# Performance work log

Measured on AMD Instinct MI355X. Metric: run time of the kernel, lower is better.

## Reference

```python
import jax, jax.numpy as jnp
import numpy as np

C = 1.0                      # Poincare ball curvature (pmath.project k=1.0)
SQRT_C = jnp.float32(np.sqrt(C))
MIN_NORM = 1e-15
BALL_EPS = 4e-3              # geoopt float32 boundary eps


def _norm(x):
    return jnp.clip(jnp.linalg.norm(x, axis=-1, keepdims=True), MIN_NORM, None)


def _artanh(x):
    return jnp.arctanh(jnp.clip(x, -1 + 1e-7, 1 - 1e-7))


def logmap0(x):
    # tangent vector at origin: artanh(sqrt(c)||x||) * x / (sqrt(c)||x||)
    n = _norm(x)
    return _artanh(SQRT_C * n) * x / (SQRT_C * n)


def expmap0(u):
    # point on ball: tanh(sqrt(c)||u||) * u / (sqrt(c)||u||)
    n = _norm(u)
    return jnp.tanh(SQRT_C * n) * u / (SQRT_C * n)


def project(x):
    # clip to open ball of radius (1-eps)/sqrt(c)
    n = _norm(x)
    maxnorm = (1.0 - BALL_EPS) / SQRT_C
    return jnp.where(n > maxnorm, x * (maxnorm / n), x)


def setup_inputs() -> dict:
    key = jax.random.key(0)
    k1, k2 = jax.random.split(key)
    B, N, D = 2, 8192, 256
    # valid Poincare-ball points: small tangent vectors mapped onto the ball
    x = project(expmap0(0.1 * jax.random.normal(k1, (B, N, D), dtype=jnp.float32)))
    # row-normalized-ish dense adjacency standing in for the sparse adj
    adj = jax.random.uniform(k2, (B, N, N), dtype=jnp.float32) / N
    return {"x": x, "adj": adj}


def reference(x, adj) -> jnp.ndarray:
    # HypAgg.forward: aggregate in tangent space at origin, map back, project
    x_tangent = logmap0(x)                          # [B, N, D]
    support_t = jnp.einsum("bij,bjd->bid", adj, x_tangent)  # batched spmm
    return project(expmap0(support_t))              # [B, N, D]
```

## Files before the change

### kernel.cpp

```cpp
#include <hip/hip_runtime.h>

#define BATCH 2
#define NN 8192
#define DD 256
#define BK 64

typedef __attribute__((ext_vector_type(8))) short bf16x8;
typedef __attribute__((ext_vector_type(4))) float f32x4;

__device__ __forceinline__ unsigned short f2bf(float f) {
    unsigned u = __builtin_bit_cast(unsigned, f);
    u += 0x7fffu + ((u >> 16) & 1u);
    return (unsigned short)(u >> 16);
}

__global__ void k_logmap_scale(const float* __restrict__ x, float* __restrict__ scale) {
    int row = blockIdx.x;
    int lane = threadIdx.x;
    const float4* xr = (const float4*)(x + (size_t)row * DD);
    float4 v = xr[lane];
    float s = v.x * v.x + v.y * v.y + v.z * v.z + v.w * v.w;
#pragma unroll
    for (int m = 1; m < 64; m <<= 1) s += __shfl_xor(s, m, 64);
    if (lane == 0) {
        float n = sqrtf(s);
        n = fmaxf(n, 1e-15f);
        float z = fminf(n, 1.0f - 1e-7f);
        float at = 0.5f * logf((1.0f + z) / (1.0f - z));
        scale[row] = at / n;
    }
}

__global__ void k_transpose(const float* __restrict__ x, const float* __restrict__ scale,
                            unsigned short* __restrict__ xtf) {
    __shared__ __align__(16) unsigned short T[DD][72];
    int bid = blockIdx.x;
    int b = bid >> 7, kb = bid & 127;
    int bn0 = b * NN + kb * 64;
    int t = threadIdx.x;
    int r = t >> 2, cc = t & 3;
    float sc = scale[bn0 + r];
    const float4* rp = (const float4*)(x + (size_t)(bn0 + r) * DD + cc * 64);
#pragma unroll
    for (int j4 = 0; j4 < 16; ++j4) {
        float4 v = rp[j4];
        int d = cc * 64 + j4 * 4;
        T[d + 0][r] = f2bf(v.x * sc);
        T[d + 1][r] = f2bf(v.y * sc);
        T[d + 2][r] = f2bf(v.z * sc);
        T[d + 3][r] = f2bf(v.w * sc);
    }
    __syncthreads();
    unsigned short* outp = xtf + (size_t)(b * 128 + kb) * DD * 64;
    int dd = t >> 3, ccc = t & 7;
#pragma unroll
    for (int p = 0; p < 8; ++p) {
        int d = dd + 32 * p;
        bf16x8 val = *(const bf16x8*)&T[d][ccc * 8];
        *(bf16x8*)(outp + (size_t)d * 64 + ccc * 8) = val;
    }
}

__global__ __launch_bounds__(256, 1) void k_gemm(const float* __restrict__ adj,
                                                 const unsigned short* __restrict__ xtf,
                                                 float* __restrict__ out) {
    __shared__ __align__(16) unsigned short A_lds[64][72];
    __shared__ float red[4][64];
    __shared__ float rowscale[64];

    int bid = blockIdx.x;
    int xcd = bid & 7;
    int b = xcd >> 2;
    int mtile = ((bid >> 3) << 2) | (xcd & 3);
    int m0 = mtile * 64;

    int t = threadIdx.x;
    int w = t >> 6, lane = t & 63, c = lane & 15, q = lane >> 4;

    int ar = t >> 4;
    int ac4 = t & 15;
    const float* abase = adj + (size_t)b * NN * NN + (size_t)(m0 + ar) * NN + ac4 * 4;

    const unsigned short* xbase = xtf + (size_t)b * 128 * DD * 64
                                + (size_t)(w * 64 + c) * 64 + q * 8;

    f32x4 acc[4][4];
#pragma unroll
    for (int i = 0; i < 4; ++i)
#pragma unroll
        for (int j = 0; j < 4; ++j)
#pragma unroll
            for (int rg = 0; rg < 4; ++rg) acc[i][j][rg] = 0.0f;

    float4 av[4];
    bf16x8 bcur[4][2], bnxt[4][2];

#pragma unroll
    for (int i = 0; i < 4; ++i)
        av[i] = *(const float4*)(abase + (size_t)(i * 16) * NN);
#pragma unroll
    for (int nt = 0; nt < 4; ++nt)
#pragma unroll
        for (int kk = 0; kk < 2; ++kk)
            bcur[nt][kk] = *(const bf16x8*)(xbase + nt * 16 * 64 + kk * 32);

    for (int kb = 0; kb < 128; ++kb) {
#pragma unroll
        for (int i = 0; i < 4; ++i) {
            ushort4 pk;
            pk.x = f2bf(av[i].x); pk.y = f2bf(av[i].y);
            pk.z = f2bf(av[i].z); pk.w = f2bf(av[i].w);
            *(ushort4*)&A_lds[ar + i * 16][ac4 * 4] = pk;
        }
        __syncthreads();

        if (kb + 1 < 128) {
            const float* ab = abase + (size_t)(kb + 1) * BK;
#pragma unroll
            for (int i = 0; i < 4; ++i)
                av[i] = *(const float4*)(ab + (size_t)(i * 16) * NN);
            const unsigned short* xb = xbase + (size_t)(kb + 1) * DD * 64;
#pragma unroll
            for (int nt = 0; nt < 4; ++nt)
#pragma unroll
                for (int kk = 0; kk < 2; ++kk)
                    bnxt[nt][kk] = *(const bf16x8*)(xb + nt * 16 * 64 + kk * 32);
        }

#pragma unroll
        for (int kk = 0; kk < 2; ++kk) {
            bf16x8 af[4];
#pragma unroll
            for (int mt = 0; mt < 4; ++mt)
                af[mt] = *(const bf16x8*)&A_lds[mt * 16 + c][kk * 32 + q * 8];
#pragma unroll
            for (int mt = 0; mt < 4; ++mt)
#pragma unroll
                for (int nt = 0; nt < 4; ++nt)
                    acc[mt][nt] = __builtin_amdgcn_mfma_f32_16x16x32_bf16(
                        af[mt], bcur[nt][kk], acc[mt][nt], 0, 0, 0);
        }
        __syncthreads();

        if (kb + 1 < 128) {
#pragma unroll
            for (int nt = 0; nt < 4; ++nt)
#pragma unroll
                for (int kk = 0; kk < 2; ++kk)
                    bcur[nt][kk] = bnxt[nt][kk];
        }
    }

    float s[4][4];
#pragma unroll
    for (int mt = 0; mt < 4; ++mt)
#pragma unroll
        for (int rg = 0; rg < 4; ++rg) {
            float v = acc[mt][0][rg] * acc[mt][0][rg] + acc[mt][1][rg] * acc[mt][1][rg]
                    + acc[mt][2][rg] * acc[mt][2][rg] + acc[mt][3][rg] * acc[mt][3][rg];
            v += __shfl_xor(v, 1, 64);
            v += __shfl_xor(v, 2, 64);
            v += __shfl_xor(v, 4, 64);
            v += __shfl_xor(v, 8, 64);
            s[mt][rg] = v;
        }
#pragma unroll
    for (int mt = 0; mt < 4; ++mt)
#pragma unroll
        for (int rg = 0; rg < 4; ++rg)
            if (c == mt * 4 + rg)
                red[w][mt * 16 + q * 4 + rg] = s[mt][rg];
    __syncthreads();
    if (t < 64) {
        float tot = red[0][t] + red[1][t] + red[2][t] + red[3][t];
        float n = sqrtf(tot);
        n = fmaxf(n, 1e-15f);
        float th = tanhf(n);
        rowscale[t] = fminf(th, 1.0f - 4e-3f) / n;
    }
    __syncthreads();

    float* obase = out + ((size_t)b * NN + m0) * DD + w * 64 + c;
#pragma unroll
    for (int mt = 0; mt < 4; ++mt)
#pragma unroll
        for (int rg = 0; rg < 4; ++rg) {
            float rs = rowscale[mt * 16 + q * 4 + rg];
            float* orow = obase + (size_t)(mt * 16 + q * 4 + rg) * DD;
#pragma unroll
            for (int nt = 0; nt < 4; ++nt)
                orow[nt * 16] = acc[mt][nt][rg] * rs;
        }
}

extern "C" void kernel_launch(void* const* d_in, const int* in_sizes, int n_in,
                              void* d_out, int out_size, void* d_ws, size_t ws_size,
                              hipStream_t stream) {
    const float* x   = (const float*)d_in[0];
    const float* adj = (const float*)d_in[1];
    float* out = (float*)d_out;

    unsigned short* xtf = (unsigned short*)d_ws;
    float* scale = (float*)((char*)d_ws + (size_t)BATCH * 128 * DD * 64 * 2);

    k_logmap_scale<<<BATCH * NN, 64, 0, stream>>>(x, scale);
    k_transpose<<<BATCH * 128, 256, 0, stream>>>(x, scale, xtf);
    k_gemm<<<256, 256, 0, stream>>>(adj, xtf, out);
}
```

Before: 801.6 us.

## Load adj directly into MFMA registers, drop LDS staging, fuse prep kernels

The GEMM no longer stages the fp32 adjacency tile through LDS with barriers. Each wave now loads its A fragments straight from global memory with nontemporal loads and converts them in registers. Waves are arranged 2x2 over a 32x128 sub-tile, and global loads are double-buffered in registers across two k-steps. The logmap norm and transpose kernels are merged into one prep kernel, and output stores are nontemporal. This removes the LDS round trips, barriers and one kernel launch, at the cost of more register pressure and less coalesced per-lane adj loads (32-byte segments per row).

```diff
diff --git a/kernel.cpp b/kernel.cpp
--- a/kernel.cpp
+++ b/kernel.cpp
@@ -3,7 +3,6 @@
 #define BATCH 2
 #define NN 8192
 #define DD 256
-#define BK 64
 
 typedef __attribute__((ext_vector_type(8))) short bf16x8;
 typedef __attribute__((ext_vector_type(4))) float f32x4;
@@ -14,41 +13,43 @@
     return (unsigned short)(u >> 16);
 }
 
-__global__ void k_logmap_scale(const float* __restrict__ x, float* __restrict__ scale) {
-    int row = blockIdx.x;
-    int lane = threadIdx.x;
-    const float4* xr = (const float4*)(x + (size_t)row * DD);
-    float4 v = xr[lane];
-    float s = v.x * v.x + v.y * v.y + v.z * v.z + v.w * v.w;
+__device__ __forceinline__ bf16x8 cvt8(f32x4 lo, f32x4 hi) {
+    bf16x8 r;
 #pragma unroll
-    for (int m = 1; m < 64; m <<= 1) s += __shfl_xor(s, m, 64);
-    if (lane == 0) {
-        float n = sqrtf(s);
-        n = fmaxf(n, 1e-15f);
-        float z = fminf(n, 1.0f - 1e-7f);
-        float at = 0.5f * logf((1.0f + z) / (1.0f - z));
-        scale[row] = at / n;
+    for (int i = 0; i < 4; ++i) {
+        r[i]     = (short)f2bf(lo[i]);
+        r[i + 4] = (short)f2bf(hi[i]);
     }
+    return r;
 }
 
-__global__ void k_transpose(const float* __restrict__ x, const float* __restrict__ scale,
-                            unsigned short* __restrict__ xtf) {
+__global__ void k_prep(const float* __restrict__ x, unsigned short* __restrict__ xtf) {
     __shared__ __align__(16) unsigned short T[DD][72];
     int bid = blockIdx.x;
     int b = bid >> 7, kb = bid & 127;
     int bn0 = b * NN + kb * 64;
     int t = threadIdx.x;
     int r = t >> 2, cc = t & 3;
-    float sc = scale[bn0 + r];
     const float4* rp = (const float4*)(x + (size_t)(bn0 + r) * DD + cc * 64);
+    float4 v[16];
+    float s = 0.0f;
 #pragma unroll
     for (int j4 = 0; j4 < 16; ++j4) {
-        float4 v = rp[j4];
+        v[j4] = rp[j4];
+        s += v[j4].x * v[j4].x + v[j4].y * v[j4].y + v[j4].z * v[j4].z + v[j4].w * v[j4].w;
+    }
+    s += __shfl_xor(s, 1, 64);
+    s += __shfl_xor(s, 2, 64);
+    float n = fmaxf(sqrtf(s), 1e-15f);
+    float z = fminf(n, 1.0f - 1e-7f);
+    float sc = (0.5f * logf((1.0f + z) / (1.0f - z))) / n;
+#pragma unroll
+    for (int j4 = 0; j4 < 16; ++j4) {
         int d = cc * 64 + j4 * 4;
-        T[d + 0][r] = f2bf(v.x * sc);
-        T[d + 1][r] = f2bf(v.y * sc);
-        T[d + 2][r] = f2bf(v.z * sc);
-        T[d + 3][r] = f2bf(v.w * sc);
+        T[d + 0][r] = f2bf(v[j4].x * sc);
+        T[d + 1][r] = f2bf(v[j4].y * sc);
+        T[d + 2][r] = f2bf(v[j4].z * sc);
+        T[d + 3][r] = f2bf(v[j4].w * sc);
     }
     __syncthreads();
     unsigned short* outp = xtf + (size_t)(b * 128 + kb) * DD * 64;
@@ -61,11 +62,46 @@
     }
 }
 
+struct ABuf { f32x4 a[2][2][2]; };
+struct BBuf { bf16x8 f[8][2]; };
+
+__device__ __forceinline__ void load_tiles(const float* abase, const unsigned short* bbase,
+                                           int kb, ABuf& A, BBuf& B) {
+#pragma unroll
+    for (int mt = 0; mt < 2; ++mt)
+#pragma unroll
+        for (int kk = 0; kk < 2; ++kk) {
+            const f32x4* p = (const f32x4*)(abase + (size_t)mt * 16 * NN + (size_t)kb * 64 + kk * 32);
+            A.a[mt][kk][0] = __builtin_nontemporal_load(p);
+            A.a[mt][kk][1] = __builtin_nontemporal_load(p + 1);
+        }
+    const unsigned short* bk = bbase + (size_t)kb * DD * 64;
+#pragma unroll
+    for (int nt = 0; nt < 8; ++nt)
+#pragma unroll
+        for (int kk = 0; kk < 2; ++kk)
+            B.f[nt][kk] = *(const bf16x8*)(bk + nt * 16 * 64 + kk * 32);
+}
+
+__device__ __forceinline__ void compute_tiles(const ABuf& A, const BBuf& B, f32x4 acc[2][8]) {
+#pragma unroll
+    for (int kk = 0; kk < 2; ++kk) {
+        bf16x8 af[2];
+#pragma unroll
+        for (int mt = 0; mt < 2; ++mt) af[mt] = cvt8(A.a[mt][kk][0], A.a[mt][kk][1]);
+#pragma unroll
+        for (int mt = 0; mt < 2; ++mt)
+#pragma unroll
+            for (int nt = 0; nt < 8; ++nt)
+                acc[mt][nt] = __builtin_amdgcn_mfma_f32_16x16x32_bf16(
+                    af[mt], B.f[nt][kk], acc[mt][nt], 0, 0, 0);
+    }
+}
+
 __global__ __launch_bounds__(256, 1) void k_gemm(const float* __restrict__ adj,
                                                  const unsigned short* __restrict__ xtf,
                                                  float* __restrict__ out) {
-    __shared__ __align__(16) unsigned short A_lds[64][72];
-    __shared__ float red[4][64];
+    __shared__ float red[2][64];
     __shared__ float rowscale[64];
 
     int bid = blockIdx.x;
@@ -76,120 +112,62 @@
 
     int t = threadIdx.x;
     int w = t >> 6, lane = t & 63, c = lane & 15, q = lane >> 4;
+    int wm = w >> 1, wn = w & 1;
 
-    int ar = t >> 4;
-    int ac4 = t & 15;
-    const float* abase = adj + (size_t)b * NN * NN + (size_t)(m0 + ar) * NN + ac4 * 4;
+    const float* abase = adj + (size_t)b * NN * NN + (size_t)(m0 + wm * 32 + c) * NN + q * 8;
+    const unsigned short* bbase = xtf + (size_t)b * 128 * DD * 64
+                                + (size_t)(wn * 128 + c) * 64 + q * 8;
 
-    const unsigned short* xbase = xtf + (size_t)b * 128 * DD * 64
-                                + (size_t)(w * 64 + c) * 64 + q * 8;
+    f32x4 acc[2][8];
+#pragma unroll
+    for (int mt = 0; mt < 2; ++mt)
+#pragma unroll
+        for (int nt = 0; nt < 8; ++nt)
+#pragma unroll
+            for (int rg = 0; rg < 4; ++rg) acc[mt][nt][rg] = 0.0f;
 
-    f32x4 acc[4][4];
-#pragma unroll
-    for (int i = 0; i < 4; ++i)
-#pragma unroll
-        for (int j = 0; j < 4; ++j)
-#pragma unroll
-            for (int rg = 0; rg < 4; ++rg) acc[i][j][rg] = 0.0f;
-
-    float4 av[4];
-    bf16x8 bcur[4][2], bnxt[4][2];
+    ABuf A0, A1;
+    BBuf B0, B1;
+    load_tiles(abase, bbase, 0, A0, B0);
+    for (int kb = 0; kb < 128; kb += 2) {
+        load_tiles(abase, bbase, kb + 1, A1, B1);
+        compute_tiles(A0, B0, acc);
+        if (kb + 2 < 128) load_tiles(abase, bbase, kb + 2, A0, B0);
+        compute_tiles(A1, B1, acc);
+    }
 
 #pragma unroll
-    for (int i = 0; i < 4; ++i)
-        av[i] = *(const float4*)(abase + (size_t)(i * 16) * NN);
-#pragma unroll
-    for (int nt = 0; nt < 4; ++nt)
-#pragma unroll
-        for (int kk = 0; kk < 2; ++kk)
-            bcur[nt][kk] = *(const bf16x8*)(xbase + nt * 16 * 64 + kk * 32);
-
-    for (int kb = 0; kb < 128; ++kb) {
-#pragma unroll
-        for (int i = 0; i < 4; ++i) {
-            ushort4 pk;
-            pk.x = f2bf(av[i].x); pk.y = f2bf(av[i].y);
-            pk.z = f2bf(av[i].z); pk.w = f2bf(av[i].w);
-            *(ushort4*)&A_lds[ar + i * 16][ac4 * 4] = pk;
-        }
-        __syncthreads();
-
-        if (kb + 1 < 128) {
-            const float* ab = abase + (size_t)(kb + 1) * BK;
-#pragma unroll
-            for (int i = 0; i < 4; ++i)
-                av[i] = *(const float4*)(ab + (size_t)(i * 16) * NN);
-            const unsigned short* xb = xbase + (size_t)(kb + 1) * DD * 64;
-#pragma unroll
-            for (int nt = 0; nt < 4; ++nt)
-#pragma unroll
-                for (int kk = 0; kk < 2; ++kk)
-                    bnxt[nt][kk] = *(const bf16x8*)(xb + nt * 16 * 64 + kk * 32);
-        }
-
-#pragma unroll
-        for (int kk = 0; kk < 2; ++kk) {
-            bf16x8 af[4];
-#pragma unroll
-            for (int mt = 0; mt < 4; ++mt)
-                af[mt] = *(const bf16x8*)&A_lds[mt * 16 + c][kk * 32 + q * 8];
-#pragma unroll
-            for (int mt = 0; mt < 4; ++mt)
-#pragma unroll
-                for (int nt = 0; nt < 4; ++nt)
-                    acc[mt][nt] = __builtin_amdgcn_mfma_f32_16x16x32_bf16(
-                        af[mt], bcur[nt][kk], acc[mt][nt], 0, 0, 0);
-        }
-        __syncthreads();
-
-        if (kb + 1 < 128) {
-#pragma unroll
-            for (int nt = 0; nt < 4; ++nt)
-#pragma unroll
-                for (int kk = 0; kk < 2; ++kk)
-                    bcur[nt][kk] = bnxt[nt][kk];
-        }
-    }
-
-    float s[4][4];
-#pragma unroll
-    for (int mt = 0; mt < 4; ++mt)
+    for (int mt = 0; mt < 2; ++mt)
 #pragma unroll
         for (int rg = 0; rg < 4; ++rg) {
-            float v = acc[mt][0][rg] * acc[mt][0][rg] + acc[mt][1][rg] * acc[mt][1][rg]
-                    + acc[mt][2][rg] * acc[mt][2][rg] + acc[mt][3][rg] * acc[mt][3][rg];
+            float v = 0.0f;
+#pragma unroll
+            for (int nt = 0; nt < 8; ++nt) v += acc[mt][nt][rg] * acc[mt][nt][rg];
             v += __shfl_xor(v, 1, 64);
             v += __shfl_xor(v, 2, 64);
             v += __shfl_xor(v, 4, 64);
             v += __shfl_xor(v, 8, 64);
-            s[mt][rg] = v;
+            if (c == 0) red[wn][wm * 32 + mt * 16 + q * 4 + rg] = v;
         }
-#pragma unroll
-    for (int mt = 0; mt < 4; ++mt)
-#pragma unroll
-        for (int rg = 0; rg < 4; ++rg)
-            if (c == mt * 4 + rg)
-                red[w][mt * 16 + q * 4 + rg] = s[mt][rg];
     __syncthreads();
     if (t < 64) {
-        float tot = red[0][t] + red[1][t] + red[2][t] + red[3][t];
-        float n = sqrtf(tot);
-        n = fmaxf(n, 1e-15f);
-        float th = tanhf(n);
-        rowscale[t] = fminf(th, 1.0f - 4e-3f) / n;
+        float tot = red[0][t] + red[1][t];
+        float n = fmaxf(sqrtf(tot), 1e-15f);
+        rowscale[t] = fminf(tanhf(n), 1.0f - 4e-3f) / n;
     }
     __syncthreads();
 
-    float* obase = out + ((size_t)b * NN + m0) * DD + w * 64 + c;
+    float* obase = out + ((size_t)(b * NN + m0 + wm * 32)) * DD + wn * 128 + c;
 #pragma unroll
-    for (int mt = 0; mt < 4; ++mt)
+    for (int mt = 0; mt < 2; ++mt)
 #pragma unroll
         for (int rg = 0; rg < 4; ++rg) {
-            float rs = rowscale[mt * 16 + q * 4 + rg];
-            float* orow = obase + (size_t)(mt * 16 + q * 4 + rg) * DD;
+            int row = mt * 16 + q * 4 + rg;
+            float rs = rowscale[wm * 32 + row];
+            float* orow = obase + (size_t)row * DD;
 #pragma unroll
-            for (int nt = 0; nt < 4; ++nt)
-                orow[nt * 16] = acc[mt][nt][rg] * rs;
+            for (int nt = 0; nt < 8; ++nt)
+                __builtin_nontemporal_store(acc[mt][nt][rg] * rs, orow + nt * 16);
         }
 }
 
@@ -201,9 +179,7 @@
     float* out = (float*)d_out;
 
     unsigned short* xtf = (unsigned short*)d_ws;
-    float* scale = (float*)((char*)d_ws + (size_t)BATCH * 128 * DD * 64 * 2);
 
-    k_logmap_scale<<<BATCH * NN, 64, 0, stream>>>(x, scale);
-    k_transpose<<<BATCH * 128, 256, 0, stream>>>(x, scale, xtf);
+    k_prep<<<BATCH * 128, 256, 0, stream>>>(x, xtf);
     k_gemm<<<256, 256, 0, stream>>>(adj, xtf, out);
 }
```

Measured after the change: 958.8 us. +19.6%, slower.
